# Optimization experiments

Measured on AMD Instinct MI355X. Metric: run time of the kernel, lower is better.

## Reference

```python
import jax, jax.numpy as jnp
import numpy as np

MAX_LEN = 8192  # static bound on per-row nonzeros (jit-friendly stand-in for data-dependent max_len)
B, D, E = 256, 65536, 128
DENSITY = 0.08  # expected nnz/row ~5243 << MAX_LEN


def setup_inputs() -> dict:
    key = jax.random.key(0)
    k1, k2, k3 = jax.random.split(key, 3)
    mask = jax.random.uniform(k1, (B, D)) < DENSITY
    x = jnp.where(mask, jax.random.normal(k2, (B, D), dtype=jnp.float32), 0.0)
    embed_table = jax.random.normal(k3, (D + 1, E), dtype=jnp.float32) * 0.02
    t = jnp.zeros((1,), dtype=jnp.float32)
    return {"t": t, "x": x, "embed_table": embed_table}


def reference(t, x, embed_table):
    # --- condense: per-row stream compaction of nonzero entries ---
    d = x.shape[1]
    mask = x != 0
    idx = jnp.arange(d)
    # push positions of zero entries to the end, keep nonzero positions sorted ascending
    keys = jnp.where(mask, idx, d)              # (B, D)
    order = jnp.sort(keys, axis=1)[:, :MAX_LEN]  # (B, MAX_LEN) compacted nonzero positions (pad = d)
    valid = order < d
    p = jnp.where(valid, order + 1, 0)           # 1-based positions, 0 = pad (matches torch code)
    v = jnp.where(valid, jnp.take_along_axis(x, jnp.minimum(order, d - 1), axis=1), 0.0)
    # --- embedding lookup on condensed positions (computed as in original; unused by output) ---
    id_embed = embed_table[p]                    # (B, MAX_LEN, E)
    # --- decondense: scatter values back to dense layout ---
    rows = jnp.arange(x.shape[0])[:, None]
    tgt = jnp.where(p > 0, p - 1, 0)
    y = jnp.zeros_like(x).at[rows, tgt].add(jnp.where(p > 0, v, 0.0))
    return y
```

## Files before the change

### kernel.cpp

```cpp
#include <hip/hip_runtime.h>

#define NROWS   256
#define DCOLS   65536
#define MAXLEN  8192
#define TPB     1024
#define EPT     (DCOLS / TPB)
#define V4PT    (EPT / 4)

__global__ __launch_bounds__(TPB) void condense_roundtrip_kernel(
        const float* __restrict__ x, float* __restrict__ y) {
    const int row  = blockIdx.x;
    const int t    = threadIdx.x;
    const int lane = t & 63;
    const int wave = t >> 6;

    const float4* __restrict__ x4 =
        reinterpret_cast<const float4*>(x + (size_t)row * DCOLS) + t * V4PT;
    float4* __restrict__ y4 =
        reinterpret_cast<float4*>(y + (size_t)row * DCOLS) + t * V4PT;

    int cnt = 0;
#pragma unroll
    for (int i = 0; i < V4PT; ++i) {
        float4 v = x4[i];
        cnt += (v.x != 0.0f) + (v.y != 0.0f) + (v.z != 0.0f) + (v.w != 0.0f);
    }

    int incl = cnt;
#pragma unroll
    for (int off = 1; off < 64; off <<= 1) {
        int n = __shfl_up(incl, off, 64);
        if (lane >= off) incl += n;
    }

    __shared__ int wsum[TPB / 64];
    __shared__ int wbase[TPB / 64];
    if (lane == 63) wsum[wave] = incl;
    __syncthreads();
    if (t == 0) {
        int acc = 0;
#pragma unroll
        for (int w = 0; w < TPB / 64; ++w) { wbase[w] = acc; acc += wsum[w]; }
    }
    __syncthreads();

    int rank = wbase[wave] + (incl - cnt);

#pragma unroll
    for (int i = 0; i < V4PT; ++i) {
        float4 v = x4[i];
        float4 o;
        bool nx = (v.x != 0.0f); o.x = (nx && rank < MAXLEN) ? v.x : 0.0f; rank += nx;
        bool ny = (v.y != 0.0f); o.y = (ny && rank < MAXLEN) ? v.y : 0.0f; rank += ny;
        bool nz = (v.z != 0.0f); o.z = (nz && rank < MAXLEN) ? v.z : 0.0f; rank += nz;
        bool nw = (v.w != 0.0f); o.w = (nw && rank < MAXLEN) ? v.w : 0.0f; rank += nw;
        y4[i] = o;
    }
}

extern "C" void kernel_launch(void* const* d_in, const int* in_sizes, int n_in,
                              void* d_out, int out_size, void* d_ws, size_t ws_size,
                              hipStream_t stream) {
    const float* x = (const float*)d_in[1];
    float* y = (float*)d_out;
    condense_roundtrip_kernel<<<NROWS, TPB, 0, stream>>>(x, y);
}
```

Measured before the change: 157.3 us.

## Add fast path copying row directly when nonzero count fits MAXLEN

Each row is loaded once into registers with a coalesced strided layout, and its nonzeros are counted with a wave xor-reduction and a block sum. If the count is at most MAXLEN, the registers are written straight to the output, skipping the second global read and the prefix-scan ranking. Rows that exceed MAXLEN fall back to the original contiguous-chunk scan path, which re-reads the row. Holding 16 float4 per thread raises register pressure, and the fast path depends on typical rows staying under the cap.

```diff
diff --git a/kernel.cpp b/kernel.cpp
--- a/kernel.cpp
+++ b/kernel.cpp
@@ -4,8 +4,8 @@
 #define DCOLS   65536
 #define MAXLEN  8192
 #define TPB     1024
-#define EPT     (DCOLS / TPB)
-#define V4PT    (EPT / 4)
+#define V4PT    16
+#define NWAVE   (TPB / 64)
 
 __global__ __launch_bounds__(TPB) void condense_roundtrip_kernel(
         const float* __restrict__ x, float* __restrict__ y) {
@@ -15,46 +15,77 @@
     const int wave = t >> 6;
 
     const float4* __restrict__ x4 =
-        reinterpret_cast<const float4*>(x + (size_t)row * DCOLS) + t * V4PT;
+        reinterpret_cast<const float4*>(x + (size_t)row * DCOLS);
     float4* __restrict__ y4 =
-        reinterpret_cast<float4*>(y + (size_t)row * DCOLS) + t * V4PT;
+        reinterpret_cast<float4*>(y + (size_t)row * DCOLS);
 
+    float4 v[V4PT];
     int cnt = 0;
 #pragma unroll
     for (int i = 0; i < V4PT; ++i) {
-        float4 v = x4[i];
-        cnt += (v.x != 0.0f) + (v.y != 0.0f) + (v.z != 0.0f) + (v.w != 0.0f);
+        v[i] = x4[i * TPB + t];
+        cnt += (v[i].x != 0.0f) + (v[i].y != 0.0f) +
+               (v[i].z != 0.0f) + (v[i].w != 0.0f);
     }
 
-    int incl = cnt;
+    int s = cnt;
+#pragma unroll
+    for (int off = 32; off; off >>= 1) s += __shfl_xor(s, off, 64);
+
+    __shared__ int wsum[NWAVE];
+    __shared__ int wbase[NWAVE];
+    __shared__ int nnz_sh;
+    if (lane == 0) wsum[wave] = s;
+    __syncthreads();
+    if (t == 0) {
+        int acc = 0;
+#pragma unroll
+        for (int w = 0; w < NWAVE; ++w) acc += wsum[w];
+        nnz_sh = acc;
+    }
+    __syncthreads();
+    const int nnz = nnz_sh;
+
+    if (nnz <= MAXLEN) {
+#pragma unroll
+        for (int i = 0; i < V4PT; ++i) y4[i * TPB + t] = v[i];
+        return;
+    }
+
+    const float4* __restrict__ xc = x4 + t * V4PT;
+    float4* __restrict__ yc = y4 + t * V4PT;
+
+    int ccnt = 0;
+#pragma unroll
+    for (int i = 0; i < V4PT; ++i) {
+        float4 w = xc[i];
+        ccnt += (w.x != 0.0f) + (w.y != 0.0f) + (w.z != 0.0f) + (w.w != 0.0f);
+    }
+    int incl = ccnt;
 #pragma unroll
     for (int off = 1; off < 64; off <<= 1) {
         int n = __shfl_up(incl, off, 64);
         if (lane >= off) incl += n;
     }
-
-    __shared__ int wsum[TPB / 64];
-    __shared__ int wbase[TPB / 64];
     if (lane == 63) wsum[wave] = incl;
     __syncthreads();
     if (t == 0) {
         int acc = 0;
 #pragma unroll
-        for (int w = 0; w < TPB / 64; ++w) { wbase[w] = acc; acc += wsum[w]; }
+        for (int w = 0; w < NWAVE; ++w) { wbase[w] = acc; acc += wsum[w]; }
     }
     __syncthreads();
-
-    int rank = wbase[wave] + (incl - cnt);
+    int rank = wbase[wave] + (incl - ccnt);
 
 #pragma unroll
     for (int i = 0; i < V4PT; ++i) {
-        float4 v = x4[i];
+        float4 w = xc[i];
         float4 o;
-        bool nx = (v.x != 0.0f); o.x = (nx && rank < MAXLEN) ? v.x : 0.0f; rank += nx;
-        bool ny = (v.y != 0.0f); o.y = (ny && rank < MAXLEN) ? v.y : 0.0f; rank += ny;
-        bool nz = (v.z != 0.0f); o.z = (nz && rank < MAXLEN) ? v.z : 0.0f; rank += nz;
-        bool nw = (v.w != 0.0f); o.w = (nw && rank < MAXLEN) ? v.w : 0.0f; rank += nw;
-        y4[i] = o;
+        bool nx = (w.x != 0.0f); o.x = (nx && rank < MAXLEN) ? w.x : 0.0f; rank += nx;
+        bool ny = (w.y != 0.0f); o.y = (ny && rank < MAXLEN) ? w.y : 0.0f; rank += ny;
+        bool nz = (w.z != 0.0f); o.z = (nz && rank < MAXLEN) ? w.z : 0.0f; rank += nz;
+        bool nw = (w.w != 0.0f); o.w = (nw && rank < MAXLEN) ? w.w : 0.0f; rank += nw;
+        yc[i] = o;
     }
 }
 
```

New measurement: 137.4 us. 12.7% less time.
